# Performance work log

Hardware: AMD Instinct MI355X
Metric: run time of the kernel (lower is better)

The kernel has to match this reference:

```python
import jax, jax.numpy as jnp
import numpy as np

T, B = 128, 64
EMB, HID, NTOK = 400, 1152, 33278
# layer dims: (in, out) per layer, matching AWD_LSTM construction
LAYER_DIMS = [(EMB, HID), (HID, HID), (HID, EMB)]


def _uniform(key, shape, bound):
    return jax.random.uniform(key, shape, jnp.float32, -bound, bound)


def setup_inputs() -> dict:
    key = jax.random.key(0)
    ks = jax.random.split(key, 32)
    inp = {
        "x": jax.random.normal(ks[0], (T, B, EMB), jnp.float32),
        "h0_0": jnp.zeros((B, HID), jnp.float32),
        "h0_1": jnp.zeros((B, HID), jnp.float32),
        "h0_2": jnp.zeros((B, EMB), jnp.float32),
        "c0_0": jnp.zeros((B, HID), jnp.float32),
        "c0_1": jnp.zeros((B, HID), jnp.float32),
        "c0_2": jnp.zeros((B, EMB), jnp.float32),
    }
    ki = 1
    for li, (din, dout) in enumerate(LAYER_DIMS):
        bound = 1.0 / np.sqrt(dout)
        inp[f"W_ih{li}"] = _uniform(ks[ki + 0], (4 * dout, din), bound)
        inp[f"W_hh{li}"] = _uniform(ks[ki + 1], (4 * dout, dout), bound)
        inp[f"b_ih{li}"] = _uniform(ks[ki + 2], (4 * dout,), bound)
        inp[f"b_hh{li}"] = _uniform(ks[ki + 3], (4 * dout,), bound)
        ki += 4
    bd = 1.0 / np.sqrt(EMB)
    inp["W_dec"] = _uniform(ks[ki], (NTOK, EMB), bd)
    inp["b_dec"] = _uniform(ks[ki + 1], (NTOK,), bd)
    return inp


def _lstm_cell(x, h, c, W_ih, W_hh, b_ih, b_hh):
    # PyTorch gate order: i, f, g, o
    gates = x @ W_ih.T + b_ih + h @ W_hh.T + b_hh
    i, f, g, o = jnp.split(gates, 4, axis=-1)
    c_new = jax.nn.sigmoid(f) * c + jax.nn.sigmoid(i) * jnp.tanh(g)
    h_new = jax.nn.sigmoid(o) * jnp.tanh(c_new)
    return h_new, c_new


def reference(x, h0_0, h0_1, h0_2, c0_0, c0_1, c0_2,
              W_ih0, W_hh0, b_ih0, b_hh0,
              W_ih1, W_hh1, b_ih1, b_hh1,
              W_ih2, W_hh2, b_ih2, b_hh2,
              W_dec, b_dec):
    params = [(W_ih0, W_hh0, b_ih0, b_hh0),
              (W_ih1, W_hh1, b_ih1, b_hh1),
              (W_ih2, W_hh2, b_ih2, b_hh2)]

    def step(carry, xt):
        hs, cs = carry
        inp = xt
        new_h, new_c = [], []
        for li in range(3):
            h, c = _lstm_cell(inp, hs[li], cs[li], *params[li])
            new_h.append(h)
            new_c.append(c)
            inp = h
        return (tuple(new_h), tuple(new_c)), new_h[-1]

    carry0 = ((h0_0, h0_1, h0_2), (c0_0, c0_1, c0_2))
    (hs, cs), out = jax.lax.scan(step, carry0, x)  # out: (T, B, EMB)
    decoded = out.reshape(T * B, EMB) @ W_dec.T + b_dec
    return decoded.reshape(T, B, NTOK)
```

## Files before the change

kernel.cpp:

```cpp
#include <hip/hip_runtime.h>
#include <math.h>

typedef unsigned short u16;
typedef unsigned int u32;
typedef __attribute__((ext_vector_type(8))) short short8;
typedef __attribute__((ext_vector_type(4))) float f32x4;
typedef __attribute__((ext_vector_type(2))) float f32x2;
typedef __attribute__((ext_vector_type(4))) unsigned int u32x4;

__device__ __forceinline__ u16 f32_to_bf16(float x) {
    union { float f; unsigned int u; } v; v.f = x;
    unsigned int u = v.u;
    return (u16)((u + 0x7FFFu + ((u >> 16) & 1u)) >> 16);
}
__device__ __forceinline__ float bf16_to_f32(u16 h) {
    union { unsigned int u; float f; } v; v.u = ((unsigned int)h) << 16; return v.f;
}

__device__ __forceinline__ void gload16v(const void* g, void* l) {
    __builtin_amdgcn_global_load_lds(
        (const __attribute__((address_space(1))) void*)g,
        (__attribute__((address_space(3))) void*)l, 16, 0, 0);
}

__device__ __forceinline__ void unpack8(u32x4 p0, u32x4 p1, short8& hv, short8& lv) {
    union { short8 v; u32 d[4]; } H, L;
    H.d[0] = __builtin_amdgcn_perm(p0[1], p0[0], 0x05040100u);
    L.d[0] = __builtin_amdgcn_perm(p0[1], p0[0], 0x07060302u);
    H.d[1] = __builtin_amdgcn_perm(p0[3], p0[2], 0x05040100u);
    L.d[1] = __builtin_amdgcn_perm(p0[3], p0[2], 0x07060302u);
    H.d[2] = __builtin_amdgcn_perm(p1[1], p1[0], 0x05040100u);
    L.d[2] = __builtin_amdgcn_perm(p1[1], p1[0], 0x07060302u);
    H.d[3] = __builtin_amdgcn_perm(p1[3], p1[2], 0x05040100u);
    L.d[3] = __builtin_amdgcn_perm(p1[3], p1[2], 0x07060302u);
    hv = H.v; lv = L.v;
}

__global__ void split_pad_kernel(const float* __restrict__ src,
                                 u16* __restrict__ hi, u16* __restrict__ lo,
                                 int N, int K, int Npad, int Kpad, int perm)
{
    int idx = blockIdx.x * 256 + threadIdx.x;
    if (idx >= Npad * Kpad) return;
    int n = idx / Kpad, k = idx - n * Kpad;
    float x = 0.f;
    if (n < N && k < K) {
        int srow = n;
        if (perm) { int dout = N >> 2; srow = (n & 3) * dout + (n >> 2); }
        x = src[(size_t)srow * K + k];
    }
    u16 h = f32_to_bf16(x);
    hi[idx] = h;
    lo[idx] = f32_to_bf16(x - bf16_to_f32(h));
}

__global__ void pack_h0_kernel(const float* __restrict__ src, u32* __restrict__ dst,
                               int Brows, int K, int Kpad)
{
    int idx = blockIdx.x * 256 + threadIdx.x;
    if (idx >= Brows * Kpad) return;
    int b = idx / Kpad, k = idx - b * Kpad;
    float x = (k < K) ? src[(size_t)b * K + k] : 0.f;
    u16 h = f32_to_bf16(x);
    u16 l = f32_to_bf16(x - bf16_to_f32(h));
    dst[idx] = (u32)h | ((u32)l << 16);
}

__global__ void zero_cols_kernel(u32* __restrict__ p, int rows, int c0, int c1, int ld)
{
    int w = c1 - c0;
    int idx = blockIdx.x * 256 + threadIdx.x;
    if (idx >= rows * w) return;
    int r = idx / w, c = idx - r * w;
    p[(size_t)r * ld + c0 + c] = 0;
}

__global__ void bias_perm_kernel(const float* __restrict__ bi,
                                 const float* __restrict__ bh,
                                 float* __restrict__ out, int N4)
{
    int c = blockIdx.x * 256 + threadIdx.x;
    if (c >= N4) return;
    int dout = N4 >> 2;
    int s = (c & 3) * dout + (c >> 2);
    out[c] = bi[s] + bh[s];
}

template<int AMODE>
__global__ __launch_bounds__(256) void gemm3m(
    const float* __restrict__ Af32,
    const u32* __restrict__ Apk,
    const u16* __restrict__ Whi, const u16* __restrict__ Wlo,
    const float* __restrict__ bias,
    float* __restrict__ C,
    int Nreal, int Kreal, int Kp, int lda, int ldc)
{
    extern __shared__ __align__(16) char smem[];
    u16 (*As)[128][32] = (u16 (*)[128][32])smem;
    u32* AsP           = (u32*)smem;
    u16 (*Ws)[128][32] = (u16 (*)[128][32])(smem + 16384);
    float (*Cs)[129]   = (float (*)[129])smem;

    const int tid  = threadIdx.x;
    const int lane = tid & 63, wave = tid >> 6;

    const int bid   = blockIdx.x;
    const int chunk = bid & 7;
    const int c     = bid >> 3;
    const int ntile = c >> 3;
    const int mtile = (chunk << 3) | (c & 7);
    const int m0 = mtile * 128, n0 = ntile * 128;

    const int wm = (wave >> 1) * 64, wn = (wave & 1) * 64;

    f32x4 acc[4][4];
#pragma unroll
    for (int i = 0; i < 4; ++i)
#pragma unroll
        for (int j = 0; j < 4; ++j)
#pragma unroll
            for (int r = 0; r < 4; ++r) acc[i][j][r] = 0.f;

    const int srow = tid >> 2;
    const int sq   = tid & 3;
    const int dq   = (sq ^ ((srow >> 2) & 3)) * 8;
    const int fr   = lane & 15;
    const int fq   = lane >> 4;
    const int rcol = (fq ^ ((fr >> 2) & 3)) * 8;
    const int lrow = lane >> 2, lq = lane & 3;

    for (int k0 = 0; k0 < Kp; k0 += 32) {
        if (AMODE == 0) {
#pragma unroll
            for (int half = 0; half < 2; ++half) {
                int row = half * 64 + srow;
                int kc  = k0 + sq * 8;
                union { u16 s[8]; short8 v; } uh, ul;
                if (kc + 8 <= Kreal) {
                    const float* p = &Af32[(size_t)(m0 + row) * lda + kc];
#pragma unroll
                    for (int j = 0; j < 8; ++j) {
                        float xv = p[j];
                        u16 hh = f32_to_bf16(xv);
                        uh.s[j] = hh;
                        ul.s[j] = f32_to_bf16(xv - bf16_to_f32(hh));
                    }
                } else {
#pragma unroll
                    for (int j = 0; j < 8; ++j) { uh.s[j] = 0; ul.s[j] = 0; }
                }
                *(short8*)&As[0][row][dq] = uh.v;
                *(short8*)&As[1][row][dq] = ul.v;
                size_t wo = (size_t)(n0 + row) * Kp + k0 + sq * 8;
                *(short8*)&Ws[0][row][dq] = *(const short8*)(Whi + wo);
                *(short8*)&Ws[1][row][dq] = *(const short8*)(Wlo + wo);
            }
        } else {
            if (wave < 2) {
                const u32* gA = Apk + (size_t)m0 * lda + k0;
#pragma unroll
                for (int g = 0; g < 8; ++g) {
                    int row = wave * 64 + g * 8 + (lane >> 3);
                    int srcc = (lane & 7) ^ (row & 7);
                    gload16v(gA + (size_t)row * lda + srcc * 4,
                             AsP + (size_t)(wave * 64 + g * 8) * 32);
                }
            } else {
                const u16* gW = ((wave == 2) ? Whi : Wlo) + (size_t)n0 * Kp + k0;
                u16* lbW = (u16*)(smem + 16384) + (wave - 2) * 4096;
#pragma unroll
                for (int g = 0; g < 8; ++g) {
                    int row = g * 16 + lrow;
                    int srcq = lq ^ ((row >> 2) & 3);
                    gload16v(gW + (size_t)row * Kp + srcq * 8, lbW + g * 512);
                }
            }
        }
        __syncthreads();

        short8 ah[4], al[4], wh[4], wl[4];
#pragma unroll
        for (int f = 0; f < 4; ++f) {
            int arow = wm + f * 16 + fr;
            if (AMODE == 0) {
                ah[f] = *(const short8*)&As[0][arow][rcol];
                al[f] = *(const short8*)&As[1][arow][rcol];
            } else {
                int s0 = (((2 * fq) ^ (arow & 7)) << 2);
                int s1 = (((2 * fq + 1) ^ (arow & 7)) << 2);
                u32x4 p0 = *(const u32x4*)&AsP[arow * 32 + s0];
                u32x4 p1 = *(const u32x4*)&AsP[arow * 32 + s1];
                unpack8(p0, p1, ah[f], al[f]);
            }
            int wrow = wn + f * 16 + fr;
            wh[f] = *(const short8*)&Ws[0][wrow][rcol];
            wl[f] = *(const short8*)&Ws[1][wrow][rcol];
        }
#pragma unroll
        for (int i = 0; i < 4; ++i)
#pragma unroll
            for (int j = 0; j < 4; ++j) {
                acc[i][j] = __builtin_amdgcn_mfma_f32_16x16x32_bf16(ah[i], wh[j], acc[i][j], 0, 0, 0);
                acc[i][j] = __builtin_amdgcn_mfma_f32_16x16x32_bf16(ah[i], wl[j], acc[i][j], 0, 0, 0);
                acc[i][j] = __builtin_amdgcn_mfma_f32_16x16x32_bf16(al[i], wh[j], acc[i][j], 0, 0, 0);
            }
        __syncthreads();
    }

    const int erow = tid & 31;
    const int echk = tid >> 5;
    const int gm_base = m0 + ((erow >> 4) * 64) + (erow & 15);
    const int gn0 = n0 + echk * 16;
    const bool vec4ok = ((ldc & 3) == 0);

#pragma unroll
    for (int i = 0; i < 4; ++i) {
        __syncthreads();
#pragma unroll
        for (int j = 0; j < 4; ++j)
#pragma unroll
            for (int r = 0; r < 4; ++r)
                Cs[(wave >> 1) * 16 + fq * 4 + r][wn + j * 16 + fr] = acc[i][j][r];
        __syncthreads();

        const int gm = gm_base + i * 16;
        float* crow = C + (size_t)gm * ldc;
        if (gn0 + 16 <= Nreal) {
#pragma unroll
            for (int q = 0; q < 4; ++q) {
                f32x4 v = *(const f32x4*)&Cs[erow][echk * 16 + q * 4];
                if (bias) {
                    f32x4 bv = *(const f32x4*)&bias[gn0 + q * 4];
                    v += bv;
                }
                if (vec4ok) {
                    *(f32x4*)&crow[gn0 + q * 4] = v;
                } else {
                    f32x2 lo2 = {v[0], v[1]}, hi2 = {v[2], v[3]};
                    *(f32x2*)&crow[gn0 + q * 4]     = lo2;
                    *(f32x2*)&crow[gn0 + q * 4 + 2] = hi2;
                }
            }
        } else {
#pragma unroll
            for (int q = 0; q < 4; ++q)
#pragma unroll
                for (int p = 0; p < 4; ++p) {
                    int n = gn0 + q * 4 + p;
                    if (n < Nreal)
                        crow[n] = Cs[erow][echk * 16 + q * 4 + p] + (bias ? bias[n] : 0.f);
                }
        }
    }
}

#define PF(S, KT_) do {                                                        \
    int q_ = (((KT_) * 4 + fq) ^ sxor) * 8;                                    \
    a0h_##S = *(const short8*)&Wlds[rA * Kp + q_];                             \
    a0l_##S = *(const short8*)&Wlds[(32 + rA) * Kp + q_];                      \
    a1h_##S = *(const short8*)&Wlds[rB * Kp + q_];                             \
    a1l_##S = *(const short8*)&Wlds[(32 + rB) * Kp + q_];                      \
    u32x4 u0_ = *(const u32x4*)(hrow + (KT_) * 32 + fq * 8);                   \
    u32x4 u1_ = *(const u32x4*)(hrow + (KT_) * 32 + fq * 8 + 4);               \
    unpack8(u0_, u1_, hh_##S, hl_##S);                                         \
} while (0)

#define CM(S) do {                                                             \
    accA = __builtin_amdgcn_mfma_f32_16x16x32_bf16(a0h_##S, hh_##S, accA, 0, 0, 0); \
    accB = __builtin_amdgcn_mfma_f32_16x16x32_bf16(a1h_##S, hh_##S, accB, 0, 0, 0); \
    accA = __builtin_amdgcn_mfma_f32_16x16x32_bf16(a0h_##S, hl_##S, accA, 0, 0, 0); \
    accB = __builtin_amdgcn_mfma_f32_16x16x32_bf16(a1h_##S, hl_##S, accB, 0, 0, 0); \
    accA = __builtin_amdgcn_mfma_f32_16x16x32_bf16(a0l_##S, hh_##S, accA, 0, 0, 0); \
    accB = __builtin_amdgcn_mfma_f32_16x16x32_bf16(a1l_##S, hh_##S, accB, 0, 0, 0); \
} while (0)

__global__ __launch_bounds__(256, 1) void persistent_lstm(
    const u16* __restrict__ Whi, const u16* __restrict__ Wlo,
    const u32* __restrict__ h0HL,
    u32* __restrict__ seqHL,
    const float* __restrict__ pre,
    const float* __restrict__ c_in, float* __restrict__ c_out,
    int* __restrict__ flags,
    int N4, int Kp, int dout, int G, int TSTEPS)
{
    extern __shared__ __align__(16) u16 Wlds[];
    const int tid  = threadIdx.x;
    const int lane = tid & 63, wave = tid >> 6;
    const int fr = lane & 15, fq = lane >> 4;
    const int c0blk = blockIdx.x * 32;
    const int CH = Kp >> 3;
    const int b = wave * 16 + fr;

    for (int idx = tid; idx < 64 * CH; idx += 256) {
        int buf = idx / (32 * CH);
        int rem = idx - buf * 32 * CH;
        int r = rem / CH, q = rem - r * CH;
        const u16* src = buf ? Wlo : Whi;
        short8 v = *(const short8*)(src + (size_t)(c0blk + r) * Kp + q * 8);
        *(short8*)&Wlds[(buf * 32 + r) * Kp + (q ^ (r & 7)) * 8] = v;
    }

    const int cA = c0blk + fq * 4;
    const int cB = cA + 16;
    const int jA = cA >> 2, jB = cB >> 2;
    float cregA = c_in[(size_t)b * dout + jA];
    float cregB = c_in[(size_t)b * dout + jB];

    const int rA = fr, rB = 16 + fr;
    const int sxor = fr & 7;
    const int KT = Kp >> 5;

    f32x4 preA = *(const f32x4*)(pre + (size_t)b * N4 + cA);
    f32x4 preB = *(const f32x4*)(pre + (size_t)b * N4 + cB);
    __syncthreads();

    for (int ts = 0; ts < TSTEPS; ++ts) {
        const u32* hbase = (ts == 0) ? h0HL : seqHL + (size_t)(ts - 1) * 64 * Kp;
        const u32* hrow = hbase + (size_t)b * Kp;

        f32x4 accA = {0.f, 0.f, 0.f, 0.f};
        f32x4 accB = {0.f, 0.f, 0.f, 0.f};
        short8 a0h_0, a0l_0, a1h_0, a1l_0, hh_0, hl_0;
        short8 a0h_1, a0l_1, a1h_1, a1l_1, hh_1, hl_1;
        short8 a0h_2, a0l_2, a1h_2, a1l_2, hh_2, hl_2;
        short8 a0h_3, a0l_3, a1h_3, a1l_3, hh_3, hl_3;
        short8 a0h_4, a0l_4, a1h_4, a1l_4, hh_4, hl_4;
        short8 a0h_5, a0l_5, a1h_5, a1l_5, hh_5, hl_5;

        PF(0, 0); PF(1, 1); PF(2, 2); PF(3, 3); PF(4, 4); PF(5, 5);
        for (int kt = 0; kt < KT - 6; kt += 6) {
            CM(0); PF(0, kt + 6);
            CM(1); PF(1, kt + 7);
            CM(2); PF(2, kt + 8);
            CM(3); PF(3, kt + 9);
            CM(4); PF(4, kt + 10);
            CM(5); PF(5, kt + 11);
        }
        CM(0); CM(1); CM(2); CM(3); CM(4); CM(5);

#pragma unroll
        for (int ct = 0; ct < 2; ++ct) {
            f32x4 a = ct ? accB : accA;
            f32x4 p = ct ? preB : preA;
            int j  = ct ? jB : jA;
            float gi = a[0] + p[0];
            float gf = a[1] + p[1];
            float gg = a[2] + p[2];
            float go_ = a[3] + p[3];
            float si = 1.f / (1.f + expf(-gi));
            float sf = 1.f / (1.f + expf(-gf));
            float so = 1.f / (1.f + expf(-go_));
            float tg = tanhf(gg);
            float cn = sf * (ct ? cregB : cregA) + si * tg;
            float hv = so * tanhf(cn);
            if (ct) cregB = cn; else cregA = cn;
            u16 hb = f32_to_bf16(hv);
            u16 lb = f32_to_bf16(hv - bf16_to_f32(hb));
            __hip_atomic_store(&seqHL[(size_t)(ts * 64 + b) * Kp + j],
                               (u32)hb | ((u32)lb << 16),
                               __ATOMIC_RELAXED, __HIP_MEMORY_SCOPE_AGENT);
        }

        if (ts != TSTEPS - 1) {
            __syncthreads();
            if (tid == 0)
                __hip_atomic_store(&flags[blockIdx.x], ts + 1,
                                   __ATOMIC_RELAXED, __HIP_MEMORY_SCOPE_AGENT);
            {
                const float* prow2 = pre + (size_t)((ts + 1) * 64 + b) * N4;
                preA = *(const f32x4*)(prow2 + cA);
                preB = *(const f32x4*)(prow2 + cB);
            }
            if (tid < G) {
                while (__hip_atomic_load(&flags[tid], __ATOMIC_RELAXED,
                                         __HIP_MEMORY_SCOPE_AGENT) < ts + 1)
                    __builtin_amdgcn_s_sleep(1);
            }
            __syncthreads();
            __builtin_amdgcn_sched_barrier(0);
        }
    }

    c_out[(size_t)b * dout + jA] = cregA;
    c_out[(size_t)b * dout + jB] = cregB;
}

extern "C" void kernel_launch(void* const* d_in, const int* in_sizes, int n_in,
                              void* d_out, int out_size, void* d_ws, size_t ws_size,
                              hipStream_t stream)
{
    const int T = 128, B = 64, EMB = 400, HID = 1152, NTOK = 33278;
    const int TB = T * B;

    const float* x     = (const float*)d_in[0];
    const float* h0[3] = {(const float*)d_in[1], (const float*)d_in[2], (const float*)d_in[3]};
    const float* c0[3] = {(const float*)d_in[4], (const float*)d_in[5], (const float*)d_in[6]};
    const float* W_ih[3] = {(const float*)d_in[7],  (const float*)d_in[11], (const float*)d_in[15]};
    const float* W_hh[3] = {(const float*)d_in[8],  (const float*)d_in[12], (const float*)d_in[16]};
    const float* b_ih[3] = {(const float*)d_in[9],  (const float*)d_in[13], (const float*)d_in[17]};
    const float* b_hh[3] = {(const float*)d_in[10], (const float*)d_in[14], (const float*)d_in[18]};
    const float* W_dec = (const float*)d_in[19];
    const float* b_dec = (const float*)d_in[20];

    const int din[3]    = {EMB, HID, HID};
    const int Kpre[3]   = {416, 1152, 1152};
    const int dh[3]     = {HID, HID, EMB};
    const int KpH[3]    = {1152, 1152, 576};
    const int N4[3]     = {4608, 4608, 1600};
    const int N4p128[3] = {4608, 4608, 1664};
    const int Gp[3]     = {144, 144, 50};

    char* wsp = (char*)d_ws;
    size_t off = 0;
    auto alloc = [&](size_t bytes) -> char* {
        char* p = wsp + off; off = (off + bytes + 255) & ~(size_t)255; return p;
    };

    float* pre   = (float*)alloc((size_t)TB * 4608 * 4);
    u32* seqHL   = (u32*)alloc((size_t)TB * 1152 * 4);
    u16* WihHi   = (u16*)alloc((size_t)4608 * 1152 * 2);
    u16* WihLo   = (u16*)alloc((size_t)4608 * 1152 * 2);
    u16* WhhHi   = (u16*)alloc((size_t)4608 * 1152 * 2);
    u16* WhhLo   = (u16*)alloc((size_t)4608 * 1152 * 2);
    u32* h0HL    = (u32*)alloc((size_t)B * 1152 * 4);
    float* bsum  = (float*)alloc(4608 * 4);
    float* cstb  = (float*)alloc((size_t)B * HID * 4);
    int* flags   = (int*)alloc(3 * 256 * 4);
    u16* WdecHi  = (u16*)pre;
    u16* WdecLo  = (u16*)pre + (size_t)33280 * 416;

    hipMemsetAsync(flags, 0, 3 * 256 * 4, stream);
    hipFuncSetAttribute(reinterpret_cast<const void*>(persistent_lstm),
                        hipFuncAttributeMaxDynamicSharedMemorySize, 160 * 1024);
    hipFuncSetAttribute(reinterpret_cast<const void*>(&gemm3m<0>),
                        hipFuncAttributeMaxDynamicSharedMemorySize, 64 * 1024);
    hipFuncSetAttribute(reinterpret_cast<const void*>(&gemm3m<2>),
                        hipFuncAttributeMaxDynamicSharedMemorySize, 64 * 1024);

    auto run_split = [&](const float* src, u16* hi, u16* lo,
                         int N, int K, int Npad, int Kpad, int perm) {
        int total = Npad * Kpad;
        split_pad_kernel<<<(total + 255) / 256, 256, 0, stream>>>(
            src, hi, lo, N, K, Npad, Kpad, perm);
    };

    for (int l = 0; l < 3; ++l) {
        run_split(W_hh[l], WhhHi, WhhLo, N4[l], dh[l], N4[l], KpH[l], 1);
        pack_h0_kernel<<<(B * KpH[l] + 255) / 256, 256, 0, stream>>>(
            h0[l], h0HL, B, dh[l], KpH[l]);
        run_split(W_ih[l], WihHi, WihLo, N4[l], din[l], N4p128[l], Kpre[l], 1);
        bias_perm_kernel<<<(N4[l] + 255) / 256, 256, 0, stream>>>(
            b_ih[l], b_hh[l], bsum, N4[l]);

        const int NT = N4p128[l] / 128;
        const size_t ldsB = (size_t)128 * KpH[l];

        if (l == 0) {
            gemm3m<0><<<dim3(NT * 64), 256, 32768, stream>>>(
                x, nullptr, WihHi, WihLo, bsum, pre,
                N4[l], EMB, Kpre[l], EMB, N4[l]);
        } else {
            gemm3m<2><<<dim3(NT * 64), 256, 32768, stream>>>(
                nullptr, seqHL, WihHi, WihLo, bsum, pre,
                N4[l], KpH[l-1], KpH[l-1], KpH[l-1], N4[l]);
        }

        persistent_lstm<<<dim3(Gp[l]), 256, ldsB, stream>>>(
            WhhHi, WhhLo, h0HL, seqHL, pre,
            c0[l], cstb, flags + l * 256,
            N4[l], KpH[l], dh[l], Gp[l], T);
    }

    zero_cols_kernel<<<(TB * 16 + 255) / 256, 256, 0, stream>>>(
        seqHL, TB, 400, 416, 576);
    run_split(W_dec, WdecHi, WdecLo, NTOK, EMB, 33280, 416, 0);
    gemm3m<2><<<dim3(260 * 64), 256, 32768, stream>>>(
        nullptr, seqHL, WdecHi, WdecLo, b_dec, (float*)d_out,
        NTOK, 416, 416, 576, NTOK);
}
```

Measured before the change: 6.102 ms.

## Replace per-step global barrier with fine-grained per-K-tile flag waits in LSTM

Removes the all-block spin barrier between timesteps of the persistent LSTM kernel. Each wave instead checks, just before loading each 32-wide K tile of h, the flags of the four producer blocks that wrote that slice, and prefetches those flags one group ahead. Blocks start their K loop at a staggered tile offset so they consume slices in different orders, which lets them begin work as soon as their first producers finish. Unused flag slots are preset to a large value so they never block. The cost is more atomic flag loads and more complex control flow in the inner loop.

```diff
diff --git a/kernel.cpp b/kernel.cpp
--- a/kernel.cpp
+++ b/kernel.cpp
@@ -254,16 +254,32 @@
     }
 }
 
-#define PF(S, KT_) do {                                                        \
-    int q_ = (((KT_) * 4 + fq) ^ sxor) * 8;                                    \
+#define PFP(S) do {                                                            \
+    if (!__all(fl##S >= ts)) {                                                 \
+        int* fp_ = flags + 4 * ktd + (lane & 3);                               \
+        do { __builtin_amdgcn_s_sleep(1);                                      \
+             fl##S = __hip_atomic_load(fp_, __ATOMIC_RELAXED,                  \
+                                       __HIP_MEMORY_SCOPE_AGENT);              \
+        } while (!__all(fl##S >= ts));                                         \
+    }                                                                          \
+    int q_ = ((ktd * 4 + fq) ^ sxor) * 8;                                      \
     a0h_##S = *(const short8*)&Wlds[rA * Kp + q_];                             \
     a0l_##S = *(const short8*)&Wlds[(32 + rA) * Kp + q_];                      \
     a1h_##S = *(const short8*)&Wlds[rB * Kp + q_];                             \
     a1l_##S = *(const short8*)&Wlds[(32 + rB) * Kp + q_];                      \
-    u32x4 u0_ = *(const u32x4*)(hrow + (KT_) * 32 + fq * 8);                   \
-    u32x4 u1_ = *(const u32x4*)(hrow + (KT_) * 32 + fq * 8 + 4);               \
+    u32x4 u0_ = *(const u32x4*)(hrow + ktd * 32 + fq * 8);                     \
+    u32x4 u1_ = *(const u32x4*)(hrow + ktd * 32 + fq * 8 + 4);                 \
     unpack8(u0_, u1_, hh_##S, hl_##S);                                         \
+    ktd = (ktd + 1 == KT) ? 0 : ktd + 1;                                       \
 } while (0)
+
+#define FLD(S) do {                                                            \
+    gl##S = __hip_atomic_load(flags + 4 * ktf + (lane & 3),                    \
+                              __ATOMIC_RELAXED, __HIP_MEMORY_SCOPE_AGENT);     \
+    ktf = (ktf + 1 == KT) ? 0 : ktf + 1;                                       \
+} while (0)
+#define FLD6 do { FLD(0); FLD(1); FLD(2); FLD(3); FLD(4); FLD(5); } while (0)
+#define SHF6 do { fl0=gl0; fl1=gl1; fl2=gl2; fl3=gl3; fl4=gl4; fl5=gl5; } while (0)
 
 #define CM(S) do {                                                             \
     accA = __builtin_amdgcn_mfma_f32_16x16x32_bf16(a0h_##S, hh_##S, accA, 0, 0, 0); \
@@ -281,7 +297,7 @@
     const float* __restrict__ pre,
     const float* __restrict__ c_in, float* __restrict__ c_out,
     int* __restrict__ flags,
-    int N4, int Kp, int dout, int G, int TSTEPS)
+    int N4, int Kp, int dout, int TSTEPS)
 {
     extern __shared__ __align__(16) u16 Wlds[];
     const int tid  = threadIdx.x;
@@ -309,6 +325,15 @@
     const int rA = fr, rB = 16 + fr;
     const int sxor = fr & 7;
     const int KT = Kp >> 5;
+    int kt0 = blockIdx.x >> 2;
+    if (kt0 >= KT) kt0 -= KT;
+
+    int ktf = kt0, ktd = kt0;
+    int fl0, fl1, fl2, fl3, fl4, fl5;
+    int gl0, gl1, gl2, gl3, gl4, gl5;
+    FLD6;
+    SHF6;
+    FLD6;
 
     f32x4 preA = *(const f32x4*)(pre + (size_t)b * N4 + cA);
     f32x4 preB = *(const f32x4*)(pre + (size_t)b * N4 + cB);
@@ -327,15 +352,18 @@
         short8 a0h_4, a0l_4, a1h_4, a1l_4, hh_4, hl_4;
         short8 a0h_5, a0l_5, a1h_5, a1l_5, hh_5, hl_5;
 
-        PF(0, 0); PF(1, 1); PF(2, 2); PF(3, 3); PF(4, 4); PF(5, 5);
-        for (int kt = 0; kt < KT - 6; kt += 6) {
-            CM(0); PF(0, kt + 6);
-            CM(1); PF(1, kt + 7);
-            CM(2); PF(2, kt + 8);
-            CM(3); PF(3, kt + 9);
-            CM(4); PF(4, kt + 10);
-            CM(5); PF(5, kt + 11);
-        }
+        PFP(0); PFP(1); PFP(2); PFP(3); PFP(4); PFP(5);
+        for (int d = 0; d < KT - 6; d += 6) {
+            SHF6;
+            if (d < KT - 12) FLD6;
+            CM(0); PFP(0);
+            CM(1); PFP(1);
+            CM(2); PFP(2);
+            CM(3); PFP(3);
+            CM(4); PFP(4);
+            CM(5); PFP(5);
+        }
+        FLD6; SHF6; FLD6;
         CM(0); CM(1); CM(2); CM(3); CM(4); CM(5);
 
 #pragma unroll
@@ -361,23 +389,15 @@
                                __ATOMIC_RELAXED, __HIP_MEMORY_SCOPE_AGENT);
         }
 
-        if (ts != TSTEPS - 1) {
-            __syncthreads();
-            if (tid == 0)
-                __hip_atomic_store(&flags[blockIdx.x], ts + 1,
-                                   __ATOMIC_RELAXED, __HIP_MEMORY_SCOPE_AGENT);
-            {
-                const float* prow2 = pre + (size_t)((ts + 1) * 64 + b) * N4;
-                preA = *(const f32x4*)(prow2 + cA);
-                preB = *(const f32x4*)(prow2 + cB);
-            }
-            if (tid < G) {
-                while (__hip_atomic_load(&flags[tid], __ATOMIC_RELAXED,
-                                         __HIP_MEMORY_SCOPE_AGENT) < ts + 1)
-                    __builtin_amdgcn_s_sleep(1);
-            }
-            __syncthreads();
-            __builtin_amdgcn_sched_barrier(0);
+        __syncthreads();
+        if (tid == 0)
+            __hip_atomic_store(&flags[blockIdx.x], ts + 1,
+                               __ATOMIC_RELAXED, __HIP_MEMORY_SCOPE_AGENT);
+        {
+            int tsn = (ts + 1 < TSTEPS) ? ts + 1 : ts;
+            const float* prow2 = pre + (size_t)(tsn * 64 + b) * N4;
+            preA = *(const f32x4*)(prow2 + cA);
+            preB = *(const f32x4*)(prow2 + cB);
         }
     }
 
@@ -430,6 +450,10 @@
     u16* WdecLo  = (u16*)pre + (size_t)33280 * 416;
 
     hipMemsetAsync(flags, 0, 3 * 256 * 4, stream);
+    for (int l = 0; l < 3; ++l)
+        hipMemsetAsync((char*)(flags + l * 256 + Gp[l]), 0x7F,
+                       (256 - Gp[l]) * 4, stream);
+
     hipFuncSetAttribute(reinterpret_cast<const void*>(persistent_lstm),
                         hipFuncAttributeMaxDynamicSharedMemorySize, 160 * 1024);
     hipFuncSetAttribute(reinterpret_cast<const void*>(&gemm3m<0>),
@@ -468,7 +492,7 @@
         persistent_lstm<<<dim3(Gp[l]), 256, ldsB, stream>>>(
             WhhHi, WhhLo, h0HL, seqHL, pre,
             c0[l], cstb, flags + l * 256,
-            N4[l], KpH[l], dh[l], Gp[l], T);
+            N4[l], KpH[l], dh[l], T);
     }
 
     zero_cols_kernel<<<(TB * 16 + 255) / 256, 256, 0, stream>>>(
```

Measured after the change: 6.550 ms. +7.3%, slower.
